# Kernel tuning notes

Hardware: AMD Instinct MI355X
Metric: run time of the kernel (lower is better)

The kernel has to match this reference:

```python
import jax, jax.numpy as jnp
import numpy as np

B, T, C = 2, 2048, 1024
H, HD = 16, 64
M = 256  # per memory bank
K_CANON = 4


def setup_inputs() -> dict:
    key = jax.random.key(0)
    ks = jax.random.split(key, 10)
    s = 0.02
    return {
        "x": jax.random.normal(ks[0], (B, T, C), jnp.float32),
        "fwd_mem": jax.random.normal(ks[1], (B, M, C), jnp.float32),
        "rev_mem": jax.random.normal(ks[2], (B, M, C), jnp.float32),
        "Wq": jax.random.normal(ks[3], (C, C), jnp.float32) * s,
        "Wk": jax.random.normal(ks[4], (C, C), jnp.float32) * s,
        "Wv": jax.random.normal(ks[5], (C, C), jnp.float32) * s,
        "Wo": jax.random.normal(ks[6], (C, C), jnp.float32) * s,
        "gate_w": jax.random.normal(ks[7], (H, C), jnp.float32) * s,
        "gate_b": jnp.zeros((H,), jnp.float32),
        "canon_w": jax.random.normal(ks[8], (C, 1, K_CANON), jnp.float32) * s,
        "canon_bias": jax.random.normal(ks[9], (C,), jnp.float32) * s,
    }


def _canon_conv(y, canon_w, canon_bias):
    # causal depthwise conv1d with residual; torch weight [C,1,K] -> WIO kernel [K,1,C]
    kern = jnp.transpose(canon_w, (2, 1, 0))
    y_pad = jnp.pad(y, ((0, 0), (K_CANON - 1, 0), (0, 0)))
    conv = jax.lax.conv_general_dilated(
        y_pad, kern, window_strides=(1,), padding='VALID',
        dimension_numbers=('NWC', 'WIO', 'NWC'), feature_group_count=C)
    return y + conv + canon_bias


def reference(x, fwd_mem, rev_mem, Wq, Wk, Wv, Wo, gate_w, gate_b, canon_w, canon_bias):
    Bn, Tn, Cn = x.shape
    scale = 1.0 / np.sqrt(HD)

    q = x @ Wq.T  # [B,T,C]
    k = x @ Wk.T
    v = x @ Wv.T
    # memory integration: project memories with same k/v proj, concat on seq dim
    k = jnp.concatenate([k, fwd_mem @ Wk.T, rev_mem @ Wk.T], axis=1)  # [B,S,C]
    v = jnp.concatenate([v, fwd_mem @ Wv.T, rev_mem @ Wv.T], axis=1)
    S = k.shape[1]
    mem_len = S - Tn

    def heads(t):
        return t.reshape(Bn, -1, H, HD).transpose(0, 2, 1, 3)  # [B,h,S,hd]

    qh, kh, vh = heads(q), heads(k), heads(v)
    scores = jnp.einsum('bhtd,bhsd->bhts', qh, kh) * scale  # [B,h,T,S]
    # causal mask over the first T key columns; memory columns fully visible
    causal = jnp.triu(jnp.ones((Tn, Tn), bool), k=1)
    full_mask = jnp.pad(causal, ((0, 0), (0, mem_len)))  # [T,S]
    scores = jnp.where(full_mask[None, None], -jnp.inf, scores)
    w = jax.nn.softmax(scores, axis=-1)

    # split chunk vs memory, gate memory contribution per head
    w_chunk, w_mem = w[..., :Tn], w[..., Tn:]
    v_chunk, v_mem = vh[:, :, :Tn], vh[:, :, Tn:]
    Y_chunk = jnp.einsum('bhts,bhsd->bhtd', w_chunk, v_chunk)
    Y_mem = jnp.einsum('bhtm,bhmd->bhtd', w_mem, v_mem)
    g = jax.nn.sigmoid(q @ gate_w.T + gate_b)  # [B,T,h]
    g = g.transpose(0, 2, 1)[..., None]  # [B,h,T,1]
    Y = Y_chunk + g * Y_mem

    attn_out = Y.transpose(0, 2, 1, 3).reshape(Bn, Tn, Cn)
    attn_out = _canon_conv(attn_out, canon_w, canon_bias)
    return attn_out @ Wo.T
```

## Files before the change

### kernel.cpp

```cpp
#include <hip/hip_runtime.h>
#include <hip/hip_bf16.h>
#include <cstdint>


typedef __bf16 bf16x8_t __attribute__((ext_vector_type(8)));
typedef __bf16 bf16x4_t __attribute__((ext_vector_type(4)));
typedef float f32x4_t __attribute__((ext_vector_type(4)));

__device__ __forceinline__ f32x4_t mfma16(bf16x8_t a, bf16x8_t b, f32x4_t c) {
    return __builtin_amdgcn_mfma_f32_16x16x32_bf16(a, b, c, 0, 0, 0);
}

__device__ __forceinline__ void gl2lds16(const void* g, void* l) {
    __builtin_amdgcn_global_load_lds(
        (__attribute__((address_space(1))) uint32_t*)(uintptr_t)g,
        (__attribute__((address_space(3))) uint32_t*)l, 16, 0, 0);
}

#define OFF_X   0
#define OFF_FWD 4194304
#define OFF_REV 4718592
#define OFF_WQ  5242880
#define OFF_WK  6291456
#define OFF_WV  7340032
#define OFF_WO  8388608
#define OFF_GW  9437184
#define OFF_GB  9453568
#define OFF_CW  9453584
#define OFF_CB  9457680
#define N_TOT   9458704

__global__ __launch_bounds__(256) void conv_all_kernel(
    const void* p0, const void* p1, const void* p2, const void* p3,
    const void* p4, const void* p5, const void* p6, const void* p7,
    const void* p8, const void* p9, const void* p10,
    __hip_bfloat16* __restrict__ arena)
{
    const int i = (blockIdx.x * 256 + threadIdx.x) * 4;
    if (i >= N_TOT) return;
    const void* src; int off;
    if      (i < OFF_FWD) { src = p0;  off = OFF_X;   }
    else if (i < OFF_REV) { src = p1;  off = OFF_FWD; }
    else if (i < OFF_WQ)  { src = p2;  off = OFF_REV; }
    else if (i < OFF_WK)  { src = p3;  off = OFF_WQ;  }
    else if (i < OFF_WV)  { src = p4;  off = OFF_WK;  }
    else if (i < OFF_WO)  { src = p5;  off = OFF_WV;  }
    else if (i < OFF_GW)  { src = p6;  off = OFF_WO;  }
    else if (i < OFF_GB)  { src = p7;  off = OFF_GW;  }
    else if (i < OFF_CW)  { src = p8;  off = OFF_GB;  }
    else if (i < OFF_CB)  { src = p9;  off = OFF_CW;  }
    else                  { src = p10; off = OFF_CB;  }
    const int j = i - off;
    const float4 f = *(const float4*)((const float*)src + j);
    arena[i + 0] = __float2bfloat16(f.x);
    arena[i + 1] = __float2bfloat16(f.y);
    arena[i + 2] = __float2bfloat16(f.z);
    arena[i + 3] = __float2bfloat16(f.w);
}

__global__ __launch_bounds__(128) void gemm_bt_kernel(
    const __hip_bfloat16* __restrict__ A, const __hip_bfloat16* __restrict__ B,
    void* __restrict__ C, int ldc, int f32o)
{
    __shared__ __align__(16) __hip_bfloat16 As[64 * 32];
    __shared__ __align__(16) __hip_bfloat16 Bs[128 * 32];
    const int tid  = threadIdx.x;
    const int lane = tid & 63;
    const int wid  = tid >> 6;
    const int q4   = lane >> 4;
    const int c16  = lane & 15;
    const int wn   = wid * 64;
    const size_t arow0 = (size_t)blockIdx.x * 64;
    const size_t brow0 = (size_t)blockIdx.y * 128;
    const int a0 = tid, a1 = tid + 128;
    const __hip_bfloat16* gA0 = A + (arow0 + (a0 >> 2)) * 1024 + ((a0 & 3) << 3);
    const __hip_bfloat16* gA1 = A + (arow0 + (a1 >> 2)) * 1024 + ((a1 & 3) << 3);
    const __hip_bfloat16* gB0 = B + (brow0 + (a0 >> 2)) * 1024 + ((a0 & 3) << 3);
    const __hip_bfloat16* gB1 = B + (brow0 + (a1 >> 2)) * 1024 + ((a1 & 3) << 3);
    const __hip_bfloat16* gB2 = B + (brow0 + ((a0 + 256) >> 2)) * 1024 + ((a0 & 3) << 3);
    const __hip_bfloat16* gB3 = B + (brow0 + ((a1 + 256) >> 2)) * 1024 + ((a1 & 3) << 3);

    f32x4_t acc[4][4];
#pragma unroll
    for (int i = 0; i < 4; ++i)
#pragma unroll
        for (int j = 0; j < 4; ++j)
#pragma unroll
            for (int r = 0; r < 4; ++r) acc[i][j][r] = 0.0f;

    for (int k0 = 0; k0 < 1024; k0 += 32) {
        gl2lds16(gA0 + k0, &As[a0 * 8]);
        gl2lds16(gA1 + k0, &As[a1 * 8]);
        gl2lds16(gB0 + k0, &Bs[a0 * 8]);
        gl2lds16(gB1 + k0, &Bs[a1 * 8]);
        gl2lds16(gB2 + k0, &Bs[(a0 + 256) * 8]);
        gl2lds16(gB3 + k0, &Bs[(a1 + 256) * 8]);
        __syncthreads();
        bf16x8_t af[4], bfr[4];
#pragma unroll
        for (int i = 0; i < 4; ++i)
            af[i] = *(const bf16x8_t*)&As[(i * 16 + c16) * 32 + q4 * 8];
#pragma unroll
        for (int j = 0; j < 4; ++j)
            bfr[j] = *(const bf16x8_t*)&Bs[(wn + j * 16 + c16) * 32 + q4 * 8];
#pragma unroll
        for (int i = 0; i < 4; ++i)
#pragma unroll
            for (int j = 0; j < 4; ++j)
                acc[i][j] = mfma16(af[i], bfr[j], acc[i][j]);
        __syncthreads();
    }
#pragma unroll
    for (int i = 0; i < 4; ++i) {
        const int mg = (int)arow0 + i * 16 + q4 * 4;
#pragma unroll
        for (int j = 0; j < 4; ++j) {
            const int ng = (int)brow0 + wn + j * 16 + c16;
#pragma unroll
            for (int r = 0; r < 4; ++r) {
                const size_t idx = (size_t)(mg + r) * ldc + ng;
                if (f32o) ((float*)C)[idx] = acc[i][j][r];
                else ((__hip_bfloat16*)C)[idx] = __float2bfloat16(acc[i][j][r]);
            }
        }
    }
}

__global__ __launch_bounds__(64) void gate_kernel(
    const __hip_bfloat16* __restrict__ QK, const __hip_bfloat16* __restrict__ gw,
    const __hip_bfloat16* __restrict__ gb, float* __restrict__ G)
{
    const int base = blockIdx.x * 16;
    const int lane = threadIdx.x;
    const int q4   = lane >> 4;
    const int c16  = lane & 15;
    f32x4_t acc = {0.0f, 0.0f, 0.0f, 0.0f};
    const __hip_bfloat16* qrow = QK + (size_t)(base + c16) * 2048 + q4 * 8;
    const __hip_bfloat16* wrow = gw + (size_t)c16 * 1024 + q4 * 8;
#pragma unroll
    for (int kk = 0; kk < 32; ++kk) {
        const bf16x8_t a = *(const bf16x8_t*)(qrow + kk * 32);
        const bf16x8_t w = *(const bf16x8_t*)(wrow + kk * 32);
        acc = mfma16(a, w, acc);
    }
    const float bias = __bfloat162float(gb[c16]);
#pragma unroll
    for (int r = 0; r < 4; ++r) {
        const int row = base + q4 * 4 + r;
        G[(size_t)row * 16 + c16] = 1.0f / (1.0f + __expf(-(acc[r] + bias)));
    }
}

#define PSTR 72
__global__ __launch_bounds__(256) void attn_kernel(
    const __hip_bfloat16* __restrict__ QK,
    const __hip_bfloat16* __restrict__ Vt,
    const float* __restrict__ G, __hip_bfloat16* __restrict__ Y)
{
    __shared__ __align__(16) __hip_bfloat16 Ks[64 * 64];
    __shared__ __align__(16) __hip_bfloat16 Vs[64 * 64];
    __shared__ __align__(16) __hip_bfloat16 Plds[4][16 * PSTR];
    const int flat = blockIdx.x;
    const int bh   = flat & 31;
    const int tIdx = 31 - (flat >> 5);
    const int b    = bh >> 4;
    const int h    = bh & 15;
    const int tid  = threadIdx.x;
    const int wid  = tid >> 6;
    const int lane = tid & 63;
    const int q4   = lane >> 4;
    const int c16  = lane & 15;
    const int rowbase = tIdx * 64 + wid * 16;

    const __hip_bfloat16* qrow = QK + (size_t)(b * 2048 + rowbase + c16) * 2048 + h * 64;
    const bf16x8_t qa0 = *(const bf16x8_t*)(qrow + q4 * 8);
    const bf16x8_t qa1 = *(const bf16x8_t*)(qrow + 32 + q4 * 8);

    float rs[4], gate[4];
    f32x4_t acc[4];
#pragma unroll
    for (int fp = 0; fp < 4; ++fp)
#pragma unroll
        for (int r = 0; r < 4; ++r) acc[fp][r] = 0.0f;
#pragma unroll
    for (int r = 0; r < 4; ++r) {
        rs[r] = 0.0f;
        gate[r] = G[(size_t)(b * 2048 + rowbase + q4 * 4 + r) * 16 + h];
    }

    const int nCausal = tIdx + 1;
    const int nTiles  = nCausal + 8;
    auto kvRow = [&](int tile) -> int {
        if (tile < nCausal) return b * 2048 + tile * 64;
        const int mi = (tile - nCausal) * 64;
        return (mi < 256) ? 4096 + b * 256 + mi : 4608 + b * 256 + (mi - 256);
    };

    const int srow0 = tid >> 3,         sch0 = (tid & 7) ^ (srow0 & 7);
    const int srow1 = (tid + 256) >> 3, sch1 = (tid & 7) ^ (srow1 & 7);
    const int sw0 = (q4 ^ (c16 & 7)) * 8;
    const int sw1 = ((q4 + 4) ^ (c16 & 7)) * 8;
    const __hip_bfloat16* Kbase = QK + 1024 + h * 64;

    for (int tile = 0; tile < nTiles; ++tile) {
        const bool isMem  = (tile >= nCausal);
        const bool isDiag = (tile == nCausal - 1);
        const int  vr     = kvRow(tile);
        __syncthreads();
        gl2lds16(Kbase + (size_t)(vr + srow0) * 2048 + sch0 * 8, &Ks[tid * 8]);
        gl2lds16(Kbase + (size_t)(vr + srow1) * 2048 + sch1 * 8, &Ks[(tid + 256) * 8]);
        gl2lds16(Vt + (size_t)(h * 64 + srow0) * 5120 + vr + sch0 * 8, &Vs[tid * 8]);
        gl2lds16(Vt + (size_t)(h * 64 + srow1) * 5120 + vr + sch1 * 8, &Vs[(tid + 256) * 8]);
        __syncthreads();
        bf16x8_t kb0[4], kb1[4], vb0[4], vb1[4];
#pragma unroll
        for (int f = 0; f < 4; ++f) {
            kb0[f] = *(const bf16x8_t*)&Ks[(f * 16 + c16) * 64 + sw0];
            kb1[f] = *(const bf16x8_t*)&Ks[(f * 16 + c16) * 64 + sw1];
            vb0[f] = *(const bf16x8_t*)&Vs[(f * 16 + c16) * 64 + sw0];
            vb1[f] = *(const bf16x8_t*)&Vs[(f * 16 + c16) * 64 + sw1];
        }
        f32x4_t sc[4];
#pragma unroll
        for (int f = 0; f < 4; ++f) {
            f32x4_t z = {0.0f, 0.0f, 0.0f, 0.0f};
            z = mfma16(qa0, kb0[f], z);
            z = mfma16(qa1, kb1[f], z);
            sc[f] = z;
        }
#pragma unroll
        for (int f = 0; f < 4; ++f)
#pragma unroll
            for (int r = 0; r < 4; ++r) {
                float p = __expf(sc[f][r] * 0.125f);
                if (isDiag) {
                    const int sg = tile * 64 + f * 16 + c16;
                    if (sg > rowbase + q4 * 4 + r) p = 0.0f;
                }
                rs[r] += p;
                if (isMem) p *= gate[r];
                Plds[wid][(q4 * 4 + r) * PSTR + f * 16 + c16] = __float2bfloat16(p);
            }
        const bf16x8_t pa0 = *(const bf16x8_t*)&Plds[wid][c16 * PSTR + q4 * 8];
        const bf16x8_t pa1 = *(const bf16x8_t*)&Plds[wid][c16 * PSTR + 32 + q4 * 8];
#pragma unroll
        for (int fp = 0; fp < 4; ++fp) {
            acc[fp] = mfma16(pa0, vb0[fp], acc[fp]);
            acc[fp] = mfma16(pa1, vb1[fp], acc[fp]);
        }
    }
#pragma unroll
    for (int m = 1; m <= 8; m <<= 1)
#pragma unroll
        for (int r = 0; r < 4; ++r) rs[r] += __shfl_xor(rs[r], m, 64);
    float inv[4];
#pragma unroll
    for (int r = 0; r < 4; ++r) inv[r] = 1.0f / rs[r];
#pragma unroll
    for (int fp = 0; fp < 4; ++fp)
#pragma unroll
        for (int r = 0; r < 4; ++r) {
            const int tg = rowbase + q4 * 4 + r;
            Y[(size_t)(b * 2048 + tg) * 1024 + h * 64 + fp * 16 + c16] =
                __float2bfloat16(acc[fp][r] * inv[r]);
        }
}

__global__ __launch_bounds__(256) void canon_kernel(
    const __hip_bfloat16* __restrict__ Yin, const __hip_bfloat16* __restrict__ cw,
    const __hip_bfloat16* __restrict__ cb, __hip_bfloat16* __restrict__ Yout)
{
    const int idx = (blockIdx.x * 256 + threadIdx.x) * 4;
    const int c = idx & 1023;
    const int t = (idx >> 10) & 2047;
    const bf16x4_t y0 = *(const bf16x4_t*)(Yin + idx);
    const bf16x4_t bb = *(const bf16x4_t*)(cb + c);
    float a[4];
#pragma unroll
    for (int i = 0; i < 4; ++i) a[i] = (float)y0[i] + (float)bb[i];
    const bf16x8_t w01 = *(const bf16x8_t*)(cw + c * 4);
    const bf16x8_t w23 = *(const bf16x8_t*)(cw + c * 4 + 8);
#pragma unroll
    for (int j = 0; j < 4; ++j) {
        if (t - 3 + j >= 0) {
            const bf16x4_t yj = *(const bf16x4_t*)(Yin + idx + (j - 3) * 1024);
            a[0] += (float)yj[0] * (float)w01[j];
            a[1] += (float)yj[1] * (float)w01[4 + j];
            a[2] += (float)yj[2] * (float)w23[j];
            a[3] += (float)yj[3] * (float)w23[4 + j];
        }
    }
    bf16x4_t o;
#pragma unroll
    for (int i = 0; i < 4; ++i) o[i] = (__bf16)a[i];
    *(bf16x4_t*)(Yout + idx) = o;
}

extern "C" void kernel_launch(void* const* d_in, const int* in_sizes, int n_in,
                              void* d_out, int out_size, void* d_ws, size_t ws_size,
                              hipStream_t stream)
{
    char* ws = (char*)d_ws;
    const size_t MB = 1ull << 20;
    if (ws_size < 50 * MB) return;

    __hip_bfloat16* arena = (__hip_bfloat16*)ws;
    __hip_bfloat16* QK    = (__hip_bfloat16*)(ws + 19 * MB);
    __hip_bfloat16* Vt    = (__hip_bfloat16*)(ws + 39 * MB);
    float*          G     = (float*)(ws + 49 * MB);
    __hip_bfloat16* Y1    = (__hip_bfloat16*)ws;
    __hip_bfloat16* Y2    = QK;

    const dim3 blk(256);
    conv_all_kernel<<<dim3((N_TOT / 4 + 255) / 256), blk, 0, stream>>>(
        d_in[0], d_in[1], d_in[2], d_in[3], d_in[4], d_in[5], d_in[6],
        d_in[7], d_in[8], d_in[9], d_in[10], arena);

    const __hip_bfloat16* xB  = arena + OFF_X;
    const __hip_bfloat16* WqB = arena + OFF_WQ;
    const __hip_bfloat16* WvB = arena + OFF_WV;
    const __hip_bfloat16* WoB = arena + OFF_WO;

    gemm_bt_kernel<<<dim3(80, 16), dim3(128), 0, stream>>>(xB,  WqB, QK, 2048, 0);
    gemm_bt_kernel<<<dim3(16, 40), dim3(128), 0, stream>>>(WvB, xB,  Vt, 5120, 0);
    gate_kernel<<<dim3(256), dim3(64), 0, stream>>>(QK, arena + OFF_GW, arena + OFF_GB, G);
    attn_kernel<<<dim3(1024), blk, 0, stream>>>(QK, Vt, G, Y1);
    canon_kernel<<<dim3(4096), blk, 0, stream>>>(Y1, arena + OFF_CW, arena + OFF_CB, Y2);
    gemm_bt_kernel<<<dim3(64, 8), dim3(128), 0, stream>>>(Y2, WoB, d_out, 1024, 1);
}
```

Baseline: 269.3 us.

## Enlarge GEMM tiles to 128x128, double-buffer LDS, and merge Q/K and V projections

The GEMM is restructured into a shared core with 128x128 block tiles, 256 threads in a 2x2 warp layout, and double-buffered LDS where the next K-slice is loaded asynchronously while the current one is computed, cutting one barrier per iteration. The QK projection and the transposed V projection are merged into a single launch that dispatches by block id. The aim is more data reuse per tile, overlap of global loads with MFMA work, and one fewer kernel launch. In exchange the grid has fewer blocks (the output GEMM drops to 256), and LDS use per block rises.

```diff
diff --git a/kernel.cpp b/kernel.cpp
--- a/kernel.cpp
+++ b/kernel.cpp
@@ -58,27 +58,24 @@
     arena[i + 3] = __float2bfloat16(f.w);
 }
 
-__global__ __launch_bounds__(128) void gemm_bt_kernel(
+__device__ __forceinline__ void gemm_core(
     const __hip_bfloat16* __restrict__ A, const __hip_bfloat16* __restrict__ B,
-    void* __restrict__ C, int ldc, int f32o)
-{
-    __shared__ __align__(16) __hip_bfloat16 As[64 * 32];
-    __shared__ __align__(16) __hip_bfloat16 Bs[128 * 32];
+    void* __restrict__ C, int ldc, int f32o, int arow0, int brow0,
+    __hip_bfloat16* As, __hip_bfloat16* Bs)
+{
     const int tid  = threadIdx.x;
     const int lane = tid & 63;
     const int wid  = tid >> 6;
     const int q4   = lane >> 4;
     const int c16  = lane & 15;
-    const int wn   = wid * 64;
-    const size_t arow0 = (size_t)blockIdx.x * 64;
-    const size_t brow0 = (size_t)blockIdx.y * 128;
-    const int a0 = tid, a1 = tid + 128;
-    const __hip_bfloat16* gA0 = A + (arow0 + (a0 >> 2)) * 1024 + ((a0 & 3) << 3);
-    const __hip_bfloat16* gA1 = A + (arow0 + (a1 >> 2)) * 1024 + ((a1 & 3) << 3);
-    const __hip_bfloat16* gB0 = B + (brow0 + (a0 >> 2)) * 1024 + ((a0 & 3) << 3);
-    const __hip_bfloat16* gB1 = B + (brow0 + (a1 >> 2)) * 1024 + ((a1 & 3) << 3);
-    const __hip_bfloat16* gB2 = B + (brow0 + ((a0 + 256) >> 2)) * 1024 + ((a0 & 3) << 3);
-    const __hip_bfloat16* gB3 = B + (brow0 + ((a1 + 256) >> 2)) * 1024 + ((a1 & 3) << 3);
+    const int wm   = (wid >> 1) * 64;
+    const int wn   = (wid & 1) * 64;
+    const int c0 = tid;
+    const int c1 = tid + 256;
+    const __hip_bfloat16* gA0 = A + (size_t)(arow0 + (c0 >> 2)) * 1024 + ((c0 & 3) << 3);
+    const __hip_bfloat16* gA1 = A + (size_t)(arow0 + (c1 >> 2)) * 1024 + ((c1 & 3) << 3);
+    const __hip_bfloat16* gB0 = B + (size_t)(brow0 + (c0 >> 2)) * 1024 + ((c0 & 3) << 3);
+    const __hip_bfloat16* gB1 = B + (size_t)(brow0 + (c1 >> 2)) * 1024 + ((c1 & 3) << 3);
 
     f32x4_t acc[4][4];
 #pragma unroll
@@ -88,34 +85,43 @@
 #pragma unroll
             for (int r = 0; r < 4; ++r) acc[i][j][r] = 0.0f;
 
-    for (int k0 = 0; k0 < 1024; k0 += 32) {
-        gl2lds16(gA0 + k0, &As[a0 * 8]);
-        gl2lds16(gA1 + k0, &As[a1 * 8]);
-        gl2lds16(gB0 + k0, &Bs[a0 * 8]);
-        gl2lds16(gB1 + k0, &Bs[a1 * 8]);
-        gl2lds16(gB2 + k0, &Bs[(a0 + 256) * 8]);
-        gl2lds16(gB3 + k0, &Bs[(a1 + 256) * 8]);
+    gl2lds16(gA0, As + c0 * 8);
+    gl2lds16(gA1, As + c1 * 8);
+    gl2lds16(gB0, Bs + c0 * 8);
+    gl2lds16(gB1, Bs + c1 * 8);
+
+    for (int it = 0; it < 32; ++it) {
+        __hip_bfloat16* curA = As + (it & 1) * 4096;
+        __hip_bfloat16* curB = Bs + (it & 1) * 4096;
         __syncthreads();
+        if (it < 31) {
+            const int nk = (it + 1) * 32;
+            __hip_bfloat16* nA = As + ((it + 1) & 1) * 4096;
+            __hip_bfloat16* nB = Bs + ((it + 1) & 1) * 4096;
+            gl2lds16(gA0 + nk, nA + c0 * 8);
+            gl2lds16(gA1 + nk, nA + c1 * 8);
+            gl2lds16(gB0 + nk, nB + c0 * 8);
+            gl2lds16(gB1 + nk, nB + c1 * 8);
+        }
         bf16x8_t af[4], bfr[4];
 #pragma unroll
         for (int i = 0; i < 4; ++i)
-            af[i] = *(const bf16x8_t*)&As[(i * 16 + c16) * 32 + q4 * 8];
+            af[i] = *(const bf16x8_t*)&curA[(wm + i * 16 + c16) * 32 + q4 * 8];
 #pragma unroll
         for (int j = 0; j < 4; ++j)
-            bfr[j] = *(const bf16x8_t*)&Bs[(wn + j * 16 + c16) * 32 + q4 * 8];
+            bfr[j] = *(const bf16x8_t*)&curB[(wn + j * 16 + c16) * 32 + q4 * 8];
 #pragma unroll
         for (int i = 0; i < 4; ++i)
 #pragma unroll
             for (int j = 0; j < 4; ++j)
                 acc[i][j] = mfma16(af[i], bfr[j], acc[i][j]);
-        __syncthreads();
     }
 #pragma unroll
     for (int i = 0; i < 4; ++i) {
-        const int mg = (int)arow0 + i * 16 + q4 * 4;
+        const int mg = arow0 + wm + i * 16 + q4 * 4;
 #pragma unroll
         for (int j = 0; j < 4; ++j) {
-            const int ng = (int)brow0 + wn + j * 16 + c16;
+            const int ng = brow0 + wn + j * 16 + c16;
 #pragma unroll
             for (int r = 0; r < 4; ++r) {
                 const size_t idx = (size_t)(mg + r) * ldc + ng;
@@ -124,6 +130,31 @@
             }
         }
     }
+}
+
+__global__ __launch_bounds__(256) void qkv_kernel(
+    const __hip_bfloat16* __restrict__ x, const __hip_bfloat16* __restrict__ Wqk,
+    const __hip_bfloat16* __restrict__ Wv,
+    __hip_bfloat16* __restrict__ QK, __hip_bfloat16* __restrict__ Vt)
+{
+    __shared__ __align__(16) __hip_bfloat16 As[2 * 128 * 32];
+    __shared__ __align__(16) __hip_bfloat16 Bs[2 * 128 * 32];
+    int id = blockIdx.x;
+    if (id < 640)
+        gemm_core(x, Wqk, QK, 2048, 0, (id >> 4) * 128, (id & 15) * 128, As, Bs);
+    else {
+        id -= 640;
+        gemm_core(Wv, x, Vt, 5120, 0, (id & 7) * 128, (id >> 3) * 128, As, Bs);
+    }
+}
+
+__global__ __launch_bounds__(256) void gemm_bt_kernel(
+    const __hip_bfloat16* __restrict__ A, const __hip_bfloat16* __restrict__ B,
+    void* __restrict__ C, int ldc, int f32o)
+{
+    __shared__ __align__(16) __hip_bfloat16 As[2 * 128 * 32];
+    __shared__ __align__(16) __hip_bfloat16 Bs[2 * 128 * 32];
+    gemm_core(A, B, C, ldc, f32o, blockIdx.x * 128, blockIdx.y * 128, As, Bs);
 }
 
 __global__ __launch_bounds__(64) void gate_kernel(
@@ -321,10 +352,9 @@
     const __hip_bfloat16* WvB = arena + OFF_WV;
     const __hip_bfloat16* WoB = arena + OFF_WO;
 
-    gemm_bt_kernel<<<dim3(80, 16), dim3(128), 0, stream>>>(xB,  WqB, QK, 2048, 0);
-    gemm_bt_kernel<<<dim3(16, 40), dim3(128), 0, stream>>>(WvB, xB,  Vt, 5120, 0);
+    qkv_kernel<<<dim3(960), blk, 0, stream>>>(xB, WqB, WvB, QK, Vt);
     gate_kernel<<<dim3(256), dim3(64), 0, stream>>>(QK, arena + OFF_GW, arena + OFF_GB, G);
     attn_kernel<<<dim3(1024), blk, 0, stream>>>(QK, Vt, G, Y1);
     canon_kernel<<<dim3(4096), blk, 0, stream>>>(Y1, arena + OFF_CW, arena + OFF_CB, Y2);
-    gemm_bt_kernel<<<dim3(64, 8), dim3(128), 0, stream>>>(Y2, WoB, d_out, 1024, 1);
-}
+    gemm_bt_kernel<<<dim3(32, 8), blk, 0, stream>>>(Y2, WoB, d_out, 1024, 1);
+}
```

After: 240.1 us. 1.12x faster.
